# Optimization experiments

Hardware: AMD Instinct MI355X
Metric: run time of the kernel (lower is better)

The kernel has to match this reference:

```python
import jax, jax.numpy as jnp
import numpy as np

C = 256
EPS = 1e-5

def layer_norm(x, g, b):
    mu = jnp.mean(x, axis=-1, keepdims=True)
    var = jnp.var(x, axis=-1, keepdims=True)
    return (x - mu) * jax.lax.rsqrt(var + EPS) * g + b

def setup_inputs() -> dict:
    key = jax.random.key(0)
    ks = jax.random.split(key, 12)
    B, H, W = 1, 64, 64
    s = 1.0 / np.sqrt(C)
    inp = {
        'lidar_features': jax.random.normal(ks[0], (B, C, H, W), jnp.float32),
        'image_features': jax.random.normal(ks[1], (B, C, H, W), jnp.float32),
        'Wq': jax.random.normal(ks[2], (C, C), jnp.float32) * s,
        'bq': jnp.zeros((C,), jnp.float32),
        'Wk': jax.random.normal(ks[3], (C, C), jnp.float32) * s,
        'bk': jnp.zeros((C,), jnp.float32),
        'Wv': jax.random.normal(ks[4], (C, C), jnp.float32) * s,
        'bv': jnp.zeros((C,), jnp.float32),
        'Wo': jax.random.normal(ks[5], (C, C), jnp.float32) * s,
        'bo': jnp.zeros((C,), jnp.float32),
        'g1': jnp.ones((C,), jnp.float32),
        'b1': jnp.zeros((C,), jnp.float32),
        'W1': jax.random.normal(ks[6], (C, 4 * C), jnp.float32) * s,
        'bf1': jnp.zeros((4 * C,), jnp.float32),
        'W2': jax.random.normal(ks[7], (4 * C, C), jnp.float32) * (1.0 / np.sqrt(4 * C)),
        'bf2': jnp.zeros((C,), jnp.float32),
        'g2': jnp.ones((C,), jnp.float32),
        'b2': jnp.zeros((C,), jnp.float32),
        'num_heads': 8,
    }
    return inp

def reference(lidar_features, image_features, Wq, bq, Wk, bk, Wv, bv, Wo, bo,
              g1, b1, W1, bf1, W2, bf2, g2, b2, num_heads):
    B, Cc, H, W = lidar_features.shape
    S = H * W
    hd = Cc // num_heads
    # [B,C,H,W] -> [B,S,C]
    x = lidar_features.reshape(B, Cc, S).transpose(0, 2, 1)
    y = image_features.reshape(B, Cc, S).transpose(0, 2, 1)
    q = x @ Wq + bq            # [B,S,C]
    k = y @ Wk + bk
    v = y @ Wv + bv
    qh = q.reshape(B, S, num_heads, hd).transpose(0, 2, 1, 3)  # [B,h,S,d]
    kh = k.reshape(B, S, num_heads, hd).transpose(0, 2, 1, 3)
    vh = v.reshape(B, S, num_heads, hd).transpose(0, 2, 1, 3)
    attn = jnp.einsum('bhqd,bhkd->bhqk', qh, kh) / jnp.sqrt(jnp.float32(hd))
    attn = jax.nn.softmax(attn, axis=-1)
    out = jnp.einsum('bhqk,bhkd->bhqd', attn, vh)
    out = out.transpose(0, 2, 1, 3).reshape(B, S, Cc)
    out = out @ Wo + bo
    # residual is the projected q in [B,S,C] layout (intended semantics)
    out = layer_norm(q + out, g1, b1)
    ffn = jax.nn.relu(out @ W1 + bf1) @ W2 + bf2
    out = layer_norm(out + ffn, g2, b2)
    return out.reshape(B, H, W, Cc).transpose(0, 3, 1, 2)
```

## Files before the change

### kernel.cpp

```cpp
#include <hip/hip_runtime.h>

#define SQ 4096
#define CCH 256
#define NH 8
#define HD 32
#define LN_EPS 1e-5f
#define NSPLIT 4
#define VROWS 48

typedef __bf16 bf16x8 __attribute__((ext_vector_type(8)));
typedef float f32x4 __attribute__((ext_vector_type(4)));
using bf16 = __bf16;

__device__ __forceinline__ float fast_exp2(float x) {
#if defined(__has_builtin)
#if __has_builtin(__builtin_amdgcn_exp2f)
    return __builtin_amdgcn_exp2f(x);
#else
    float r;
    asm("v_exp_f32 %0, %1" : "=v"(r) : "v"(x));
    return r;
#endif
#else
    float r;
    asm("v_exp_f32 %0, %1" : "=v"(r) : "v"(x));
    return r;
#endif
}

__device__ __forceinline__ void tile_tc(const float* __restrict__ src, bf16* __restrict__ dst,
                                        int R, int Ccol, int ti, int tj) {
    __shared__ float t[32][33];
    const int tx = threadIdx.x & 31;
    const int ty = threadIdx.x >> 5;
    const int i0 = ti * 32, j0 = tj * 32;
    #pragma unroll
    for (int i = 0; i < 32; i += 8)
        t[ty + i][tx] = src[(size_t)(i0 + ty + i) * Ccol + j0 + tx];
    __syncthreads();
    #pragma unroll
    for (int i = 0; i < 32; i += 8)
        dst[(size_t)(j0 + ty + i) * R + i0 + tx] = (bf16)t[tx][ty + i];
}

__global__ __launch_bounds__(256)
void cvt_all(const float* __restrict__ x, const float* __restrict__ y,
             bf16* __restrict__ xT, bf16* __restrict__ yT,
             const float* Wq, const float* Wk, const float* Wv, const float* Wo,
             const float* W1, const float* W2,
             bf16* WqT, bf16* WkT, bf16* WvT, bf16* WoT, bf16* W1T, bf16* W2T,
             bf16* vTb) {
    const int id = blockIdx.x;
    if (id < 2048) {
        const int z = id >> 10;
        const int t = id & 1023;
        const float* s = z ? y : x;
        bf16* d = z ? yT : xT;
        tile_tc(s, d, CCH, SQ, t >> 7, t & 127);
        return;
    }
    const int wid = id - 2048;
    if (wid < 256) {
        const int w = wid >> 6, local = wid & 63;
        const float* s = (w == 0) ? Wq : (w == 1) ? Wk : (w == 2) ? Wv : Wo;
        bf16* d = (w == 0) ? WqT : (w == 1) ? WkT : (w == 2) ? WvT : WoT;
        tile_tc(s, d, 256, 256, local >> 3, local & 7);
    } else if (wid < 512) {
        const int local = wid - 256;
        tile_tc(W1, W1T, 256, 1024, local >> 5, local & 31);
    } else if (wid < 768) {
        const int local = wid - 512;
        tile_tc(W2, W2T, 1024, 256, local >> 3, local & 7);
    } else {
        const int local = wid - 768;
        #pragma unroll
        for (int rr = 0; rr < 2; ++rr) {
            const int pr = local * 2 + rr;
            const int hh = pr >> 4, j = pr & 15;
            const bf16 val = (bf16)((j == 0) ? 1.0f : 0.0f);
            bf16x8 v8;
            #pragma unroll
            for (int e = 0; e < 8; ++e) v8[e] = val;
            bf16* dst = vTb + ((size_t)hh * VROWS + 32 + j) * SQ + threadIdx.x * 16;
            *reinterpret_cast<bf16x8*>(dst) = v8;
            *reinterpret_cast<bf16x8*>(dst + 8) = v8;
        }
    }
}

template <int K, int OUT_MODE, bool RELU>
__global__ __launch_bounds__(256)
void gemm_mfma(const bf16* __restrict__ A, const bf16* __restrict__ BT,
               const float* __restrict__ bias, float* __restrict__ Cf,
               bf16* __restrict__ Cb, int N) {
    const int tid = threadIdx.x;
    const int w = tid >> 6, l = tid & 63;
    const int l15 = l & 15, lg = l >> 4;
    const int m0 = blockIdx.x * 64 + (w >> 1) * 32;
    const int n0 = blockIdx.y * 64 + (w & 1) * 32;

    f32x4 acc[2][2] = {};
    const bf16* a0 = &A[(size_t)(m0 + l15) * K + lg * 8];
    const bf16* b0 = &BT[(size_t)(n0 + l15) * K + lg * 8];

    for (int k0 = 0; k0 < K; k0 += 32) {
        bf16x8 a[2], b[2];
        a[0] = *reinterpret_cast<const bf16x8*>(a0 + k0);
        a[1] = *reinterpret_cast<const bf16x8*>(a0 + (size_t)16 * K + k0);
        b[0] = *reinterpret_cast<const bf16x8*>(b0 + k0);
        b[1] = *reinterpret_cast<const bf16x8*>(b0 + (size_t)16 * K + k0);
        #pragma unroll
        for (int i = 0; i < 2; ++i)
            #pragma unroll
            for (int j = 0; j < 2; ++j)
                acc[i][j] = __builtin_amdgcn_mfma_f32_16x16x32_bf16(a[i], b[j], acc[i][j], 0, 0, 0);
    }

    #pragma unroll
    for (int i = 0; i < 2; ++i) {
        #pragma unroll
        for (int j = 0; j < 2; ++j) {
            const int col = n0 + j * 16 + l15;
            const float bs = bias[col];
            #pragma unroll
            for (int r = 0; r < 4; ++r) {
                const int row = m0 + i * 16 + lg * 4 + r;
                float val = acc[i][j][r] + bs;
                if (RELU) val = fmaxf(val, 0.f);
                if constexpr (OUT_MODE == 0)
                    Cf[(size_t)row * N + col] = val;
                if constexpr (OUT_MODE == 2)
                    Cb[(size_t)row * N + col] = (bf16)val;
            }
        }
    }
}

template <int K, int KS>
__global__ __launch_bounds__(256)
void gemm_sk(const bf16* __restrict__ A, const bf16* __restrict__ BT,
             const float* __restrict__ bias, float* __restrict__ Cf, int N) {
    constexpr int KSL = K / KS;
    const int z = blockIdx.z;
    const int tid = threadIdx.x;
    const int w = tid >> 6, l = tid & 63;
    const int l15 = l & 15, lg = l >> 4;
    const int m0 = blockIdx.x * 64 + (w >> 1) * 32;
    const int n0 = blockIdx.y * 64 + (w & 1) * 32;

    f32x4 acc[2][2] = {};
    const bf16* a0 = &A[(size_t)(m0 + l15) * K + z * KSL + lg * 8];
    const bf16* b0 = &BT[(size_t)(n0 + l15) * K + z * KSL + lg * 8];

    for (int k0 = 0; k0 < KSL; k0 += 32) {
        bf16x8 a[2], b[2];
        a[0] = *reinterpret_cast<const bf16x8*>(a0 + k0);
        a[1] = *reinterpret_cast<const bf16x8*>(a0 + (size_t)16 * K + k0);
        b[0] = *reinterpret_cast<const bf16x8*>(b0 + k0);
        b[1] = *reinterpret_cast<const bf16x8*>(b0 + (size_t)16 * K + k0);
        #pragma unroll
        for (int i = 0; i < 2; ++i)
            #pragma unroll
            for (int j = 0; j < 2; ++j)
                acc[i][j] = __builtin_amdgcn_mfma_f32_16x16x32_bf16(a[i], b[j], acc[i][j], 0, 0, 0);
    }

    float* C = Cf + (size_t)z * SQ * N;
    #pragma unroll
    for (int i = 0; i < 2; ++i) {
        #pragma unroll
        for (int j = 0; j < 2; ++j) {
            const int col = n0 + j * 16 + l15;
            const float bs = (z == 0) ? bias[col] : 0.f;
            #pragma unroll
            for (int r = 0; r < 4; ++r) {
                const int row = m0 + i * 16 + lg * 4 + r;
                C[(size_t)row * N + col] = acc[i][j][r] + bs;
            }
        }
    }
}

__global__ __launch_bounds__(256)
void qkv_gemm(const bf16* __restrict__ xT, const bf16* __restrict__ yT,
              const bf16* __restrict__ WqT, const bf16* __restrict__ WkT,
              const bf16* __restrict__ WvT,
              const float* __restrict__ bq, const float* __restrict__ bk,
              const float* __restrict__ bv,
              bf16* __restrict__ qb, bf16* __restrict__ kbb, bf16* __restrict__ vTb,
              float kscale) {
    const int z = blockIdx.z;
    const bf16* A  = (z == 0) ? xT : yT;
    const bf16* BT = (z == 0) ? WqT : (z == 1) ? WkT : WvT;
    const float* bias = (z == 0) ? bq : (z == 1) ? bk : bv;

    const int tid = threadIdx.x;
    const int w = tid >> 6, l = tid & 63;
    const int l15 = l & 15, lg = l >> 4;
    const int m0 = blockIdx.x * 64 + (w >> 1) * 32;
    const int n0 = blockIdx.y * 64 + (w & 1) * 32;

    f32x4 acc[2][2] = {};
    const bf16* a0 = &A[(size_t)(m0 + l15) * CCH + lg * 8];
    const bf16* b0 = &BT[(size_t)(n0 + l15) * CCH + lg * 8];

    for (int k0 = 0; k0 < CCH; k0 += 32) {
        bf16x8 a[2], b[2];
        a[0] = *reinterpret_cast<const bf16x8*>(a0 + k0);
        a[1] = *reinterpret_cast<const bf16x8*>(a0 + (size_t)16 * CCH + k0);
        b[0] = *reinterpret_cast<const bf16x8*>(b0 + k0);
        b[1] = *reinterpret_cast<const bf16x8*>(b0 + (size_t)16 * CCH + k0);
        #pragma unroll
        for (int i = 0; i < 2; ++i)
            #pragma unroll
            for (int j = 0; j < 2; ++j)
                acc[i][j] = __builtin_amdgcn_mfma_f32_16x16x32_bf16(a[i], b[j], acc[i][j], 0, 0, 0);
    }

    const float sc = (z == 1) ? kscale : 1.f;
    #pragma unroll
    for (int i = 0; i < 2; ++i) {
        #pragma unroll
        for (int j = 0; j < 2; ++j) {
            const int col = n0 + j * 16 + l15;
            const float bs = bias[col];
            #pragma unroll
            for (int r = 0; r < 4; ++r) {
                const int row = m0 + i * 16 + lg * 4 + r;
                float val = acc[i][j][r] + bs;
                if (z == 2)
                    vTb[((size_t)(col >> 5) * VROWS + (col & 31)) * SQ + row] = (bf16)val;
                else if (z == 1)
                    kbb[(size_t)row * CCH + col] = (bf16)(val * sc);
                else
                    qb[(size_t)row * CCH + col] = (bf16)val;
            }
        }
    }
}

__global__ __launch_bounds__(256)
void wo_ln1(const bf16* __restrict__ atb, const bf16* __restrict__ WoT,
            const float* __restrict__ bo, const bf16* __restrict__ qb,
            const float* __restrict__ g, const float* __restrict__ beta,
            float* __restrict__ ln1, bf16* __restrict__ ln1b) {
    const int tid = threadIdx.x;
    const int w = tid >> 6, l = tid & 63;
    const int l15 = l & 15, lg = l >> 4;
    const int mr = blockIdx.x * 16;
    const int n0 = w * 64;

    f32x4 acc[4] = {};
    const bf16* a0 = &atb[(size_t)(mr + l15) * CCH + lg * 8];
    const bf16* b0 = &WoT[(size_t)(n0 + l15) * CCH + lg * 8];
    #pragma unroll
    for (int k0 = 0; k0 < CCH; k0 += 32) {
        bf16x8 a = *reinterpret_cast<const bf16x8*>(a0 + k0);
        #pragma unroll
        for (int j = 0; j < 4; ++j) {
            bf16x8 b = *reinterpret_cast<const bf16x8*>(b0 + (size_t)j * 16 * CCH + k0);
            acc[j] = __builtin_amdgcn_mfma_f32_16x16x32_bf16(a, b, acc[j], 0, 0, 0);
        }
    }

    float val[4][4];
    float rsum[4] = {0.f, 0.f, 0.f, 0.f}, rsq[4] = {0.f, 0.f, 0.f, 0.f};
    #pragma unroll
    for (int j = 0; j < 4; ++j) {
        const int col = n0 + j * 16 + l15;
        const float bs = bo[col];
        #pragma unroll
        for (int r = 0; r < 4; ++r) {
            const int row = mr + lg * 4 + r;
            float v = acc[j][r] + bs + (float)qb[(size_t)row * CCH + col];
            val[j][r] = v;
            rsum[r] += v;
            rsq[r] += v * v;
        }
    }
    #pragma unroll
    for (int r = 0; r < 4; ++r) {
        #pragma unroll
        for (int off = 1; off < 16; off <<= 1) {
            rsum[r] += __shfl_xor(rsum[r], off);
            rsq[r]  += __shfl_xor(rsq[r], off);
        }
    }
    __shared__ float ssum[4][16], ssq[4][16];
    if (l15 == 0) {
        #pragma unroll
        for (int r = 0; r < 4; ++r) {
            ssum[w][lg * 4 + r] = rsum[r];
            ssq[w][lg * 4 + r]  = rsq[r];
        }
    }
    __syncthreads();
    float mu_[4], rs_[4];
    #pragma unroll
    for (int r = 0; r < 4; ++r) {
        const int row = lg * 4 + r;
        float s = (ssum[0][row] + ssum[1][row]) + (ssum[2][row] + ssum[3][row]);
        float q = (ssq[0][row] + ssq[1][row]) + (ssq[2][row] + ssq[3][row]);
        float mu = s * (1.0f / CCH);
        float var = q * (1.0f / CCH) - mu * mu;
        mu_[r] = mu;
        rs_[r] = rsqrtf(var + LN_EPS);
    }
    #pragma unroll
    for (int j = 0; j < 4; ++j) {
        const int col = n0 + j * 16 + l15;
        const float gg = g[col], bb = beta[col];
        #pragma unroll
        for (int r = 0; r < 4; ++r) {
            const int row = mr + lg * 4 + r;
            float res = (val[j][r] - mu_[r]) * rs_[r] * gg + bb;
            ln1[(size_t)row * CCH + col] = res;
            ln1b[(size_t)row * CCH + col] = (bf16)res;
        }
    }
}

__global__ __launch_bounds__(256)
void flash_attn11(const bf16* __restrict__ qb, const bf16* __restrict__ kb,
                  const bf16* __restrict__ vT, bf16* __restrict__ Op,
                  float* __restrict__ Lp) {
    const int fid = blockIdx.x + 16 * (blockIdx.y + NH * blockIdx.z);
    const int nid = (fid & 7) * 64 + (fid >> 3);
    const int q0 = (nid & 15) * 256;
    const int h  = (nid >> 4) & 7;
    const int sp = nid >> 7;

    const int tid = threadIdx.x;
    const int w = tid >> 6, l = tid & 63;
    const int l15 = l & 15, lg = l >> 4;

    __shared__ unsigned int Sb[4][2][8][72];

    bf16x8 aq[4];
    #pragma unroll
    for (int su = 0; su < 4; ++su)
        aq[su] = *reinterpret_cast<const bf16x8*>(
            &qb[(size_t)(q0 + su * 64 + w * 16 + l15) * CCH + h * HD + lg * 8]);

    f32x4 o[4][2] = {};
    f32x4 o2[4] = {};

    const bf16* kfrag = &kb[(size_t)l15 * CCH + h * HD + lg * 8];
    const bf16* vfrag = &vT[((size_t)h * VROWS + l15) * SQ + lg * 8];

    const int kt0 = sp * (SQ / NSPLIT / 64);
    const int kt1 = kt0 + (SQ / NSPLIT / 64);

    for (int kt = kt0; kt < kt1; ++kt) {
        const int kb0 = kt * 64;

        bf16x8 kf[4], vf[3][2];
        #pragma unroll
        for (int t = 0; t < 4; ++t)
            kf[t] = *reinterpret_cast<const bf16x8*>(kfrag + (size_t)(kb0 + t * 16) * CCH);
        #pragma unroll
        for (int dh = 0; dh < 3; ++dh)
            #pragma unroll
            for (int kh = 0; kh < 2; ++kh)
                vf[dh][kh] = *reinterpret_cast<const bf16x8*>(
                    vfrag + (size_t)dh * 16 * SQ + kb0 + kh * 32);

        #pragma unroll
        for (int su = 0; su < 4; ++su) {
            const int par = su & 1;
            f32x4 s[4];
            #pragma unroll
            for (int t = 0; t < 4; ++t)
                s[t] = __builtin_amdgcn_mfma_f32_16x16x32_bf16(
                    kf[t], aq[su], (f32x4){0.f, 0.f, 0.f, 0.f}, 0, 0, 0);

            #pragma unroll
            for (int t = 0; t < 4; ++t) {
                unsigned int u0 = __builtin_bit_cast(unsigned int, fast_exp2(s[t][0]));
                unsigned int u1 = __builtin_bit_cast(unsigned int, fast_exp2(s[t][1]));
                unsigned int u2 = __builtin_bit_cast(unsigned int, fast_exp2(s[t][2]));
                unsigned int u3 = __builtin_bit_cast(unsigned int, fast_exp2(s[t][3]));
                Sb[w][par][t * 2 + 0][l] = __builtin_amdgcn_perm(u1, u0, 0x07060302u);
                Sb[w][par][t * 2 + 1][l] = __builtin_amdgcn_perm(u3, u2, 0x07060302u);
            }

            #pragma unroll
            for (int kh = 0; kh < 2; ++kh) {
                const int sbase = kh * 4 + (lg >> 1) * 2;
                const int i0 = l15 + 16 * ((lg & 1) * 2);
                const int i1 = i0 + 16;
                union { unsigned int u[4]; bf16x8 v; } pb;
                pb.u[0] = Sb[w][par][sbase + 0][i0];
                pb.u[1] = Sb[w][par][sbase + 1][i0];
                pb.u[2] = Sb[w][par][sbase + 0][i1];
                pb.u[3] = Sb[w][par][sbase + 1][i1];
                #pragma unroll
                for (int dh = 0; dh < 2; ++dh)
                    o[su][dh] = __builtin_amdgcn_mfma_f32_16x16x32_bf16(
                        vf[dh][kh], pb.v, o[su][dh], 0, 0, 0);
                o2[su] = __builtin_amdgcn_mfma_f32_16x16x32_bf16(
                    vf[2][kh], pb.v, o2[su], 0, 0, 0);
            }
        }
    }

    const size_t obase = ((size_t)sp * NH + h) * HD;
    #pragma unroll
    for (int su = 0; su < 4; ++su) {
        const int qrow = q0 + su * 64 + w * 16 + l15;
        #pragma unroll
        for (int dh = 0; dh < 2; ++dh)
            #pragma unroll
            for (int r = 0; r < 4; ++r)
                Op[(obase + dh * 16 + lg * 4 + r) * SQ + qrow] = (bf16)o[su][dh][r];
        if (lg == 0)
            Lp[((size_t)sp * NH + h) * SQ + qrow] = o2[su][0];
    }
}

__global__ __launch_bounds__(256)
void attn_merge3(const bf16* __restrict__ Op, const float* __restrict__ Lp,
                 bf16* __restrict__ atb) {
    const int h = blockIdx.y;
    const int q0 = blockIdx.x * 64;
    const int t = threadIdx.x;
    __shared__ float sInv[64];
    __shared__ float trans[32][65];

    if (t < 64) {
        float L = 0.f;
        #pragma unroll
        for (int sp = 0; sp < NSPLIT; ++sp)
            L += Lp[((size_t)sp * NH + h) * SQ + q0 + t];
        sInv[t] = 1.0f / L;
    }
    __syncthreads();

    const int q = t & 63, dg = t >> 6;
    float a[8] = {0.f, 0.f, 0.f, 0.f, 0.f, 0.f, 0.f, 0.f};
    for (int sp = 0; sp < NSPLIT; ++sp) {
        const size_t rb = ((size_t)sp * NH + h) * HD;
        #pragma unroll
        for (int i = 0; i < 8; ++i) {
            const int d = i * 4 + dg;
            a[i] += (float)Op[(rb + d) * SQ + q0 + q];
        }
    }
    const float invq = sInv[q];
    #pragma unroll
    for (int i = 0; i < 8; ++i)
        trans[i * 4 + dg][q] = a[i] * invq;
    __syncthreads();

    const int oq = t >> 2, od = (t & 3) * 8;
    bf16x8 o8;
    #pragma unroll
    for (int j = 0; j < 8; ++j) o8[j] = (bf16)trans[od + j][oq];
    *reinterpret_cast<bf16x8*>(&atb[(size_t)(q0 + oq) * CCH + h * HD + od]) = o8;
}

__global__ __launch_bounds__(256)
void add_ln_t(const float* __restrict__ a, const float* __restrict__ b,
              const float* __restrict__ g, const float* __restrict__ beta,
              float* __restrict__ out) {
    const int s0 = blockIdx.x * 32;
    const int t = threadIdx.x;
    const int row = t >> 3;
    const int e8 = t & 7;
    const size_t base = (size_t)(s0 + row) * CCH + e8 * 32;
    const size_t PS = (size_t)SQ * CCH;

    float v[32];
    float sum = 0.f, sq = 0.f;
    #pragma unroll
    for (int j = 0; j < 32; j += 4) {
        float4 va = *reinterpret_cast<const float4*>(&a[base + j]);
        float4 vb = *reinterpret_cast<const float4*>(&b[base + j]);
        float4 vc = *reinterpret_cast<const float4*>(&b[base + PS + j]);
        v[j]     = va.x + vb.x + vc.x;
        v[j + 1] = va.y + vb.y + vc.y;
        v[j + 2] = va.z + vb.z + vc.z;
        v[j + 3] = va.w + vb.w + vc.w;
        sum += (v[j] + v[j + 1]) + (v[j + 2] + v[j + 3]);
        sq  += (v[j] * v[j] + v[j + 1] * v[j + 1]) + (v[j + 2] * v[j + 2] + v[j + 3] * v[j + 3]);
    }
    sum += __shfl_xor(sum, 1); sum += __shfl_xor(sum, 2); sum += __shfl_xor(sum, 4);
    sq  += __shfl_xor(sq, 1);  sq  += __shfl_xor(sq, 2);  sq  += __shfl_xor(sq, 4);
    const float mu = sum * (1.0f / CCH);
    const float var = sq * (1.0f / CCH) - mu * mu;
    const float rs = rsqrtf(var + LN_EPS);
    #pragma unroll
    for (int j = 0; j < 32; j += 4) {
        float4 gg = *reinterpret_cast<const float4*>(&g[e8 * 32 + j]);
        float4 bb = *reinterpret_cast<const float4*>(&beta[e8 * 32 + j]);
        v[j]     = (v[j]     - mu) * rs * gg.x + bb.x;
        v[j + 1] = (v[j + 1] - mu) * rs * gg.y + bb.y;
        v[j + 2] = (v[j + 2] - mu) * rs * gg.z + bb.z;
        v[j + 3] = (v[j + 3] - mu) * rs * gg.w + bb.w;
    }

    __shared__ float tile[32][33];
    const int cl = t >> 3, f4 = (t & 7) * 4;
    for (int c = 0; c < 8; ++c) {
        __syncthreads();
        if (e8 == c) {
            #pragma unroll
            for (int j = 0; j < 32; ++j) tile[j][row] = v[j];
        }
        __syncthreads();
        float4 o4 = {tile[cl][f4], tile[cl][f4 + 1], tile[cl][f4 + 2], tile[cl][f4 + 3]};
        *reinterpret_cast<float4*>(&out[(size_t)(c * 32 + cl) * SQ + s0 + f4]) = o4;
    }
}

extern "C" void kernel_launch(void* const* d_in, const int* in_sizes, int n_in,
                              void* d_out, int out_size, void* d_ws, size_t ws_size,
                              hipStream_t stream) {
    const float* lidar = (const float*)d_in[0];
    const float* image = (const float*)d_in[1];
    const float* Wq  = (const float*)d_in[2];
    const float* bq  = (const float*)d_in[3];
    const float* Wk  = (const float*)d_in[4];
    const float* bk  = (const float*)d_in[5];
    const float* Wv  = (const float*)d_in[6];
    const float* bv  = (const float*)d_in[7];
    const float* Wo  = (const float*)d_in[8];
    const float* bo  = (const float*)d_in[9];
    const float* g1  = (const float*)d_in[10];
    const float* b1  = (const float*)d_in[11];
    const float* W1  = (const float*)d_in[12];
    const float* bf1 = (const float*)d_in[13];
    const float* W2  = (const float*)d_in[14];
    const float* bf2 = (const float*)d_in[15];
    const float* g2  = (const float*)d_in[16];
    const float* b2  = (const float*)d_in[17];
    float* out = (float*)d_out;

    char* ws = (char*)d_ws;
    const size_t KB = 1024;
    bf16* W2T = (bf16*)(ws + 0);
    bf16* W1T = (bf16*)(ws + 512 * KB);
    bf16* WoT = (bf16*)(ws + 1024 * KB);
    bf16* WqT = (bf16*)(ws + 1152 * KB);
    bf16* WkT = (bf16*)(ws + 1280 * KB);
    bf16* WvT = (bf16*)(ws + 1408 * KB);
    bf16* qb  = (bf16*)(ws + 1536 * KB);
    bf16* kbb = (bf16*)(ws + 3584 * KB);
    bf16* vTb = (bf16*)(ws + 5632 * KB);
    bf16* xT  = (bf16*)(ws + 8704 * KB);
    bf16* yT  = (bf16*)(ws + 10752 * KB);
    bf16* Op  = (bf16*)(ws + 8704 * KB);
    float* Lp = (float*)d_out;
    bf16* atb = (bf16*)(ws + 3584 * KB);
    float* ln1 = (float*)(ws + 19968 * KB);
    bf16* ln1b = (bf16*)(ws + 5632 * KB);
    bf16* h1  = (bf16*)(ws + 9728 * KB);
    float* h2 = (float*)(ws + 1536 * KB);

    const float qscale = 0.17677669529663687f * 1.4426950408889634f;
    dim3 blk(256);

    cvt_all<<<dim3(2880), blk, 0, stream>>>(lidar, image, xT, yT,
                                            Wq, Wk, Wv, Wo, W1, W2,
                                            WqT, WkT, WvT, WoT, W1T, W2T, vTb);
    qkv_gemm<<<dim3(64, 4, 3), blk, 0, stream>>>(xT, yT, WqT, WkT, WvT,
                                                 bq, bk, bv, qb, kbb, vTb, qscale);
    flash_attn11<<<dim3(SQ / 256, NH, NSPLIT), blk, 0, stream>>>(qb, kbb, vTb, Op, Lp);
    attn_merge3<<<dim3(SQ / 64, NH), blk, 0, stream>>>(Op, Lp, atb);
    wo_ln1<<<dim3(SQ / 16), blk, 0, stream>>>(atb, WoT, bo, qb, g1, b1, ln1, ln1b);
    gemm_mfma<256, 2, true><<<dim3(64, 16), blk, 0, stream>>>(ln1b, W1T, bf1, nullptr, h1, 1024);
    gemm_sk<1024, 2><<<dim3(64, 4, 2), blk, 0, stream>>>(h1, W2T, bf2, h2, 256);
    add_ln_t<<<dim3(SQ / 32), blk, 0, stream>>>(ln1, h2, g2, b2, out);
}
```

Measured before the change: 128.7 us.

## Fuse FFN second GEMM with residual LayerNorm and transposed store

Replaces the split-K W2 GEMM and the separate add+LayerNorm+transpose kernel with one kernel. Each block computes 16 rows across all 256 output channels, adds bias and the ln1 residual, reduces LayerNorm statistics through shuffles and shared memory, then writes the result transposed. This removes the fp32 h2 partial-sum round trip through global memory and one launch. In exchange it drops split-K, so each block walks the full K=1024 and the grid falls to 256 blocks with a 16-row tile, which lowers parallelism and W2 reuse per block.

```diff
diff --git a/kernel.cpp b/kernel.cpp
--- a/kernel.cpp
+++ b/kernel.cpp
@@ -136,51 +136,6 @@
     }
 }
 
-template <int K, int KS>
-__global__ __launch_bounds__(256)
-void gemm_sk(const bf16* __restrict__ A, const bf16* __restrict__ BT,
-             const float* __restrict__ bias, float* __restrict__ Cf, int N) {
-    constexpr int KSL = K / KS;
-    const int z = blockIdx.z;
-    const int tid = threadIdx.x;
-    const int w = tid >> 6, l = tid & 63;
-    const int l15 = l & 15, lg = l >> 4;
-    const int m0 = blockIdx.x * 64 + (w >> 1) * 32;
-    const int n0 = blockIdx.y * 64 + (w & 1) * 32;
-
-    f32x4 acc[2][2] = {};
-    const bf16* a0 = &A[(size_t)(m0 + l15) * K + z * KSL + lg * 8];
-    const bf16* b0 = &BT[(size_t)(n0 + l15) * K + z * KSL + lg * 8];
-
-    for (int k0 = 0; k0 < KSL; k0 += 32) {
-        bf16x8 a[2], b[2];
-        a[0] = *reinterpret_cast<const bf16x8*>(a0 + k0);
-        a[1] = *reinterpret_cast<const bf16x8*>(a0 + (size_t)16 * K + k0);
-        b[0] = *reinterpret_cast<const bf16x8*>(b0 + k0);
-        b[1] = *reinterpret_cast<const bf16x8*>(b0 + (size_t)16 * K + k0);
-        #pragma unroll
-        for (int i = 0; i < 2; ++i)
-            #pragma unroll
-            for (int j = 0; j < 2; ++j)
-                acc[i][j] = __builtin_amdgcn_mfma_f32_16x16x32_bf16(a[i], b[j], acc[i][j], 0, 0, 0);
-    }
-
-    float* C = Cf + (size_t)z * SQ * N;
-    #pragma unroll
-    for (int i = 0; i < 2; ++i) {
-        #pragma unroll
-        for (int j = 0; j < 2; ++j) {
-            const int col = n0 + j * 16 + l15;
-            const float bs = (z == 0) ? bias[col] : 0.f;
-            #pragma unroll
-            for (int r = 0; r < 4; ++r) {
-                const int row = m0 + i * 16 + lg * 4 + r;
-                C[(size_t)row * N + col] = acc[i][j][r] + bs;
-            }
-        }
-    }
-}
-
 __global__ __launch_bounds__(256)
 void qkv_gemm(const bf16* __restrict__ xT, const bf16* __restrict__ yT,
               const bf16* __restrict__ WqT, const bf16* __restrict__ WkT,
@@ -317,6 +272,93 @@
             ln1[(size_t)row * CCH + col] = res;
             ln1b[(size_t)row * CCH + col] = (bf16)res;
         }
+    }
+}
+
+__global__ __launch_bounds__(256)
+void ffn2_ln2_t(const bf16* __restrict__ h1, const bf16* __restrict__ W2T,
+                const float* __restrict__ bf2, const float* __restrict__ ln1,
+                const float* __restrict__ g, const float* __restrict__ beta,
+                float* __restrict__ out) {
+    const int tid = threadIdx.x;
+    const int w = tid >> 6, l = tid & 63;
+    const int l15 = l & 15, lg = l >> 4;
+    const int mr = blockIdx.x * 16;
+    const int n0 = w * 64;
+
+    f32x4 acc[4] = {};
+    const bf16* a0 = &h1[(size_t)(mr + l15) * 1024 + lg * 8];
+    const bf16* b0 = &W2T[(size_t)(n0 + l15) * 1024 + lg * 8];
+    for (int k0 = 0; k0 < 1024; k0 += 32) {
+        bf16x8 a = *reinterpret_cast<const bf16x8*>(a0 + k0);
+        #pragma unroll
+        for (int j = 0; j < 4; ++j) {
+            bf16x8 b = *reinterpret_cast<const bf16x8*>(b0 + (size_t)j * 16 * 1024 + k0);
+            acc[j] = __builtin_amdgcn_mfma_f32_16x16x32_bf16(a, b, acc[j], 0, 0, 0);
+        }
+    }
+
+    float val[4][4];
+    float rsum[4] = {0.f, 0.f, 0.f, 0.f}, rsq[4] = {0.f, 0.f, 0.f, 0.f};
+    #pragma unroll
+    for (int j = 0; j < 4; ++j) {
+        const int col = n0 + j * 16 + l15;
+        const float bs = bf2[col];
+        #pragma unroll
+        for (int r = 0; r < 4; ++r) {
+            const int row = mr + lg * 4 + r;
+            float v = acc[j][r] + bs + ln1[(size_t)row * CCH + col];
+            val[j][r] = v;
+            rsum[r] += v;
+            rsq[r] += v * v;
+        }
+    }
+    #pragma unroll
+    for (int r = 0; r < 4; ++r) {
+        #pragma unroll
+        for (int off = 1; off < 16; off <<= 1) {
+            rsum[r] += __shfl_xor(rsum[r], off);
+            rsq[r]  += __shfl_xor(rsq[r], off);
+        }
+    }
+    __shared__ float ssum[4][16], ssq[4][16];
+    if (l15 == 0) {
+        #pragma unroll
+        for (int r = 0; r < 4; ++r) {
+            ssum[w][lg * 4 + r] = rsum[r];
+            ssq[w][lg * 4 + r]  = rsq[r];
+        }
+    }
+    __syncthreads();
+    float mu_[4], rs_[4];
+    #pragma unroll
+    for (int r = 0; r < 4; ++r) {
+        const int row = lg * 4 + r;
+        float s = (ssum[0][row] + ssum[1][row]) + (ssum[2][row] + ssum[3][row]);
+        float q = (ssq[0][row] + ssq[1][row]) + (ssq[2][row] + ssq[3][row]);
+        float mu = s * (1.0f / CCH);
+        float var = q * (1.0f / CCH) - mu * mu;
+        mu_[r] = mu;
+        rs_[r] = rsqrtf(var + LN_EPS);
+    }
+
+    __shared__ float tile[256][17];
+    #pragma unroll
+    for (int j = 0; j < 4; ++j) {
+        const int col = n0 + j * 16 + l15;
+        const float gg = g[col], bb = beta[col];
+        #pragma unroll
+        for (int r = 0; r < 4; ++r)
+            tile[col][lg * 4 + r] = (val[j][r] - mu_[r]) * rs_[r] * gg + bb;
+    }
+    __syncthreads();
+    const int c = tid;
+    float* orow = &out[(size_t)c * SQ + mr];
+    #pragma unroll
+    for (int q4 = 0; q4 < 4; ++q4) {
+        float4 o4 = {tile[c][q4 * 4], tile[c][q4 * 4 + 1],
+                     tile[c][q4 * 4 + 2], tile[c][q4 * 4 + 3]};
+        *reinterpret_cast<float4*>(orow + q4 * 4) = o4;
     }
 }
 
@@ -457,60 +499,6 @@
     #pragma unroll
     for (int j = 0; j < 8; ++j) o8[j] = (bf16)trans[od + j][oq];
     *reinterpret_cast<bf16x8*>(&atb[(size_t)(q0 + oq) * CCH + h * HD + od]) = o8;
-}
-
-__global__ __launch_bounds__(256)
-void add_ln_t(const float* __restrict__ a, const float* __restrict__ b,
-              const float* __restrict__ g, const float* __restrict__ beta,
-              float* __restrict__ out) {
-    const int s0 = blockIdx.x * 32;
-    const int t = threadIdx.x;
-    const int row = t >> 3;
-    const int e8 = t & 7;
-    const size_t base = (size_t)(s0 + row) * CCH + e8 * 32;
-    const size_t PS = (size_t)SQ * CCH;
-
-    float v[32];
-    float sum = 0.f, sq = 0.f;
-    #pragma unroll
-    for (int j = 0; j < 32; j += 4) {
-        float4 va = *reinterpret_cast<const float4*>(&a[base + j]);
-        float4 vb = *reinterpret_cast<const float4*>(&b[base + j]);
-        float4 vc = *reinterpret_cast<const float4*>(&b[base + PS + j]);
-        v[j]     = va.x + vb.x + vc.x;
-        v[j + 1] = va.y + vb.y + vc.y;
-        v[j + 2] = va.z + vb.z + vc.z;
-        v[j + 3] = va.w + vb.w + vc.w;
-        sum += (v[j] + v[j + 1]) + (v[j + 2] + v[j + 3]);
-        sq  += (v[j] * v[j] + v[j + 1] * v[j + 1]) + (v[j + 2] * v[j + 2] + v[j + 3] * v[j + 3]);
-    }
-    sum += __shfl_xor(sum, 1); sum += __shfl_xor(sum, 2); sum += __shfl_xor(sum, 4);
-    sq  += __shfl_xor(sq, 1);  sq  += __shfl_xor(sq, 2);  sq  += __shfl_xor(sq, 4);
-    const float mu = sum * (1.0f / CCH);
-    const float var = sq * (1.0f / CCH) - mu * mu;
-    const float rs = rsqrtf(var + LN_EPS);
-    #pragma unroll
-    for (int j = 0; j < 32; j += 4) {
-        float4 gg = *reinterpret_cast<const float4*>(&g[e8 * 32 + j]);
-        float4 bb = *reinterpret_cast<const float4*>(&beta[e8 * 32 + j]);
-        v[j]     = (v[j]     - mu) * rs * gg.x + bb.x;
-        v[j + 1] = (v[j + 1] - mu) * rs * gg.y + bb.y;
-        v[j + 2] = (v[j + 2] - mu) * rs * gg.z + bb.z;
-        v[j + 3] = (v[j + 3] - mu) * rs * gg.w + bb.w;
-    }
-
-    __shared__ float tile[32][33];
-    const int cl = t >> 3, f4 = (t & 7) * 4;
-    for (int c = 0; c < 8; ++c) {
-        __syncthreads();
-        if (e8 == c) {
-            #pragma unroll
-            for (int j = 0; j < 32; ++j) tile[j][row] = v[j];
-        }
-        __syncthreads();
-        float4 o4 = {tile[cl][f4], tile[cl][f4 + 1], tile[cl][f4 + 2], tile[cl][f4 + 3]};
-        *reinterpret_cast<float4*>(&out[(size_t)(c * 32 + cl) * SQ + s0 + f4]) = o4;
-    }
 }
 
 extern "C" void kernel_launch(void* const* d_in, const int* in_sizes, int n_in,
@@ -555,7 +543,6 @@
     float* ln1 = (float*)(ws + 19968 * KB);
     bf16* ln1b = (bf16*)(ws + 5632 * KB);
     bf16* h1  = (bf16*)(ws + 9728 * KB);
-    float* h2 = (float*)(ws + 1536 * KB);
 
     const float qscale = 0.17677669529663687f * 1.4426950408889634f;
     dim3 blk(256);
@@ -569,6 +556,5 @@
     attn_merge3<<<dim3(SQ / 64, NH), blk, 0, stream>>>(Op, Lp, atb);
     wo_ln1<<<dim3(SQ / 16), blk, 0, stream>>>(atb, WoT, bo, qb, g1, b1, ln1, ln1b);
     gemm_mfma<256, 2, true><<<dim3(64, 16), blk, 0, stream>>>(ln1b, W1T, bf1, nullptr, h1, 1024);
-    gemm_sk<1024, 2><<<dim3(64, 4, 2), blk, 0, stream>>>(h1, W2T, bf2, h2, 256);
-    add_ln_t<<<dim3(SQ / 32), blk, 0, stream>>>(ln1, h2, g2, b2, out);
-}
+    ffn2_ln2_t<<<dim3(SQ / 16), blk, 0, stream>>>(h1, W2T, bf2, ln1, g2, b2, out);
+}
```

Result: faster. 120.6 us (-6.3%).
